# Performance work log

Hardware: AMD Instinct MI355X
Metric: run time of the kernel (lower is better)

## Reference

```python
import math
import jax, jax.numpy as jnp
import numpy as np

N_HEADS = 16


def setup_inputs() -> dict:
    key = jax.random.key(0)
    qkv = jax.random.normal(key, (4, 3072, 2048), dtype=jnp.float32)
    return {"qkv": qkv}


def reference(qkv) -> jnp.ndarray:
    bs, width, length = qkv.shape
    assert width % (3 * N_HEADS) == 0
    ch = width // (3 * N_HEADS)
    # [bs*H, 3*ch, T] -> q, k, v each [bs*H, ch, T]
    qkv_r = qkv.reshape(bs * N_HEADS, 3 * ch, length)
    q, k, v = qkv_r[:, :ch], qkv_r[:, ch:2 * ch], qkv_r[:, 2 * ch:]
    scale = 1.0 / math.sqrt(math.sqrt(ch))
    # scores: [bs*H, T, T]
    weight = jnp.einsum('bct,bcs->bts', q * scale, k * scale)
    weight = jax.nn.softmax(weight.astype(jnp.float32), axis=-1).astype(weight.dtype)
    a = jnp.einsum('bts,bcs->bct', weight, v)  # [bs*H, ch, T]
    return a.reshape(bs, N_HEADS * ch, length)
```

## Files before the change

kernel.cpp:

```cpp
#include <hip/hip_runtime.h>
#include <hip/hip_bf16.h>
#include <cstdint>
#include <cstddef>

typedef short bf16x8 __attribute__((ext_vector_type(8)));
typedef float f32x16 __attribute__((ext_vector_type(16)));
typedef unsigned int uint2v __attribute__((ext_vector_type(2)));

#define QSCALE 0.18033688011112043f

__device__ __forceinline__ short f2bf(float f) {
  union { __hip_bfloat16 b; short s; } u;
  u.b = __float2bfloat16(f);
  return u.s;
}

__device__ __forceinline__ float exp2v(float x) {
  float r;
  asm("v_exp_f32 %0, %1" : "=v"(r) : "v"(x));
  return r;
}

__device__ __forceinline__ unsigned int packbf2(float a, float b) {
  union { __hip_bfloat162 h; unsigned int w; } u;
  u.h = __float22bfloat162_rn(float2{a, b});
  return u.w;
}

__device__ __forceinline__ unsigned int fbits(float f) {
  union { float f; unsigned int u; } x; x.f = f; return x.u;
}
__device__ __forceinline__ float bfloat(unsigned int u) {
  union { unsigned int u; float f; } x; x.u = u; return x.f;
}

__device__ __forceinline__ float fmax_x32(float v) {
  const uint2v r = __builtin_amdgcn_permlane32_swap(fbits(v), fbits(v),
                                                    false, false);
  return fmaxf(bfloat(r[0]), bfloat(r[1]));
}
__device__ __forceinline__ float fadd_x32(float v) {
  const uint2v r = __builtin_amdgcn_permlane32_swap(fbits(v), fbits(v),
                                                    false, false);
  return bfloat(r[0]) + bfloat(r[1]);
}

__device__ __forceinline__ void gload16(const short* g, char* l) {
  __builtin_amdgcn_global_load_lds(
      (const __attribute__((address_space(1))) void*)g,
      (__attribute__((address_space(3))) void*)l, 16, 0, 0);
}

__global__ __launch_bounds__(256, 4) void qkv_prep_kernel(
    const float* __restrict__ qkv, short* __restrict__ Kt,
    short* __restrict__ Vb) {
  const int bh = blockIdx.x >> 5;
  const int s0 = (blockIdx.x & 31) << 6;
  const int tid = threadIdx.x;
  const int row = tid >> 2;
  const int part = tid & 3;
  __shared__ float lds[64 * 65];

  const size_t qb = (size_t)bh * (192 * 2048);

  {
    const float* src = qkv + qb + (size_t)(64 + row) * 2048 + s0 + part * 16;
#pragma unroll
    for (int k4 = 0; k4 < 4; ++k4) {
      float4 v = ((const float4*)src)[k4];
      float* p = &lds[row * 65 + part * 16 + k4 * 4];
      p[0] = v.x; p[1] = v.y; p[2] = v.z; p[3] = v.w;
    }
  }
  __syncthreads();
  {
    bf16x8 o0, o1;
#pragma unroll
    for (int k = 0; k < 8; ++k) o0[k] = f2bf(lds[(part * 16 + k) * 65 + row]);
#pragma unroll
    for (int k = 0; k < 8; ++k) o1[k] = f2bf(lds[(part * 16 + 8 + k) * 65 + row]);
    short* dst = Kt + ((size_t)bh * 2048 + s0 + row) * 64 + part * 16;
    *(bf16x8*)dst = o0;
    *(bf16x8*)(dst + 8) = o1;
  }
  {
    const float* src = qkv + qb + (size_t)(128 + row) * 2048 + s0 + part * 16;
    float a[16];
#pragma unroll
    for (int k4 = 0; k4 < 4; ++k4) {
      float4 v = ((const float4*)src)[k4];
      a[k4 * 4 + 0] = v.x; a[k4 * 4 + 1] = v.y;
      a[k4 * 4 + 2] = v.z; a[k4 * 4 + 3] = v.w;
    }
    bf16x8 o0, o1;
#pragma unroll
    for (int k = 0; k < 8; ++k) { o0[k] = f2bf(a[k]); o1[k] = f2bf(a[8 + k]); }
    short* dst = Vb + ((size_t)bh * 64 + row) * 2048 + s0 + part * 16;
    *(bf16x8*)dst = o0;
    *(bf16x8*)(dst + 8) = o1;
  }
}

__global__ __launch_bounds__(512, 4) void attn32_kernel(
    const float* __restrict__ qkv, const short* __restrict__ Kt,
    const short* __restrict__ Vb, float* __restrict__ out) {
  const int bid = blockIdx.x;
  const int vid = (bid & 7) * 64 + (bid >> 3);
  const int bh = vid >> 3;
  const int tblk = vid & 7;
  const int tid = threadIdx.x;
  const int wv = tid >> 6;
  const int lane = tid & 63;
  const int tl = lane & 31;
  const int hi = lane >> 5;
  const int t0w = tblk * 256 + wv * 32;

  __shared__ __align__(16) char smem[32768];

  const size_t qb = (size_t)bh * (192 * 2048);
  bf16x8 qf[4];
#pragma unroll
  for (int kc = 0; kc < 4; ++kc) {
#pragma unroll
    for (int j = 0; j < 8; ++j) {
      const int c = kc * 16 + hi * 8 + j;
      qf[kc][j] = f2bf(qkv[qb + (size_t)c * 2048 + t0w + tl] * QSCALE);
    }
  }

  f32x16 zv;
#pragma unroll
  for (int r = 0; r < 16; ++r) zv[r] = 0.f;

  f32x16 acc[2];
#pragma unroll
  for (int cb = 0; cb < 2; ++cb) acc[cb] = zv;

  float mrun = -1e30f;
  float lsum = 0.f;

  const int rsw = (tl & 7) * 16;
  int off[2][4];
#pragma unroll
  for (int x = 0; x < 2; ++x)
#pragma unroll
    for (int j = 0; j < 4; ++j)
      off[x][j] = (x * 32 + tl) * 128 + ((j * 32 + hi * 16) ^ rsw);

  const int srow = tid >> 3;
  const int sl = tid & 7;
  const short* kg = Kt + (size_t)bh * (2048 * 64) + (size_t)srow * 64 +
                    ((sl ^ (srow & 7)) * 8);
  const short* vg = Vb + ((size_t)bh * 64 + srow) * 2048 +
                    ((sl ^ (srow & 7)) * 8);
  const int ldb = wv * 1024;

  gload16(kg, smem + ldb);
  gload16(vg, smem + 8192 + ldb);

#pragma unroll 2
  for (int ch = 0; ch < 32; ++ch) {
    char* const Kls = smem + (ch & 1) * 16384;
    char* const Vls = Kls + 8192;

    __syncthreads();

    if (ch < 31) {
      char* const Knx = smem + ((ch + 1) & 1) * 16384;
      gload16(kg + (size_t)(ch + 1) * 4096, Knx + ldb);
      gload16(vg + (ch + 1) * 64, Knx + 8192 + ldb);
    }

    __builtin_amdgcn_s_setprio(1);
    f32x16 lg[2];
#pragma unroll
    for (int st = 0; st < 2; ++st) {
      bf16x8 ka = *(const bf16x8*)(Kls + off[st][0]);
      lg[st] = __builtin_amdgcn_mfma_f32_32x32x16_bf16(ka, qf[0], zv, 0, 0, 0);
#pragma unroll
      for (int kc = 1; kc < 4; ++kc) {
        ka = *(const bf16x8*)(Kls + off[st][kc]);
        lg[st] = __builtin_amdgcn_mfma_f32_32x32x16_bf16(ka, qf[kc], lg[st],
                                                         0, 0, 0);
      }
    }
    __builtin_amdgcn_s_setprio(0);

    float w[11];
#pragma unroll
    for (int i = 0; i < 5; ++i)
      w[i] = fmaxf(fmaxf(lg[0][3 * i], lg[0][3 * i + 1]), lg[0][3 * i + 2]);
    w[5] = fmaxf(fmaxf(lg[0][15], lg[1][0]), lg[1][1]);
#pragma unroll
    for (int i = 0; i < 4; ++i)
      w[6 + i] = fmaxf(fmaxf(lg[1][3 * i + 2], lg[1][3 * i + 3]),
                       lg[1][3 * i + 4]);
    w[10] = fmaxf(lg[1][14], lg[1][15]);
    const float x0 = fmaxf(fmaxf(w[0], w[1]), w[2]);
    const float x1 = fmaxf(fmaxf(w[3], w[4]), w[5]);
    const float x2 = fmaxf(fmaxf(w[6], w[7]), w[8]);
    const float x3 = fmaxf(w[9], w[10]);
    float cm = fmax_x32(fmaxf(fmaxf(x0, x1), fmaxf(x2, x3)));
    if (!__all(cm <= mrun + 8.0f)) {
      const float nm = fmaxf(mrun, cm);
      const float fac = exp2v(mrun - nm);
      mrun = nm;
      lsum *= fac;
#pragma unroll
      for (int cb = 0; cb < 2; ++cb)
#pragma unroll
        for (int r = 0; r < 16; ++r) acc[cb][r] *= fac;
    }

    float ps = 0.f;
#pragma unroll
    for (int st = 0; st < 2; ++st) {
#pragma unroll
      for (int r = 0; r < 16; ++r) lg[st][r] = exp2v(lg[st][r] - mrun);
#pragma unroll
      for (int r = 0; r < 8; ++r) ps += lg[st][2 * r] + lg[st][2 * r + 1];
    }
    lsum += ps;

    bf16x8 pa[4];
#pragma unroll
    for (int st = 0; st < 2; ++st) {
#pragma unroll
      for (int kl = 0; kl < 2; ++kl) {
        const unsigned int p0a = packbf2(lg[st][8 * kl + 0], lg[st][8 * kl + 1]);
        const unsigned int p0b = packbf2(lg[st][8 * kl + 2], lg[st][8 * kl + 3]);
        const unsigned int p1a = packbf2(lg[st][8 * kl + 4], lg[st][8 * kl + 5]);
        const unsigned int p1b = packbf2(lg[st][8 * kl + 6], lg[st][8 * kl + 7]);
        const unsigned int sa = hi ? p0a : p1a;
        const unsigned int sb = hi ? p0b : p1b;
        const unsigned int ra = __shfl_xor(sa, 32);
        const unsigned int rb = __shfl_xor(sb, 32);
        union { unsigned int w[4]; bf16x8 v; } u;
        u.w[0] = hi ? ra : p0a;
        u.w[1] = hi ? rb : p0b;
        u.w[2] = hi ? p1a : ra;
        u.w[3] = hi ? p1b : rb;
        pa[st * 2 + kl] = u.v;
      }
    }

    __builtin_amdgcn_s_setprio(1);
#pragma unroll
    for (int cb = 0; cb < 2; ++cb) {
#pragma unroll
      for (int ks = 0; ks < 4; ++ks) {
        const bf16x8 vb = *(const bf16x8*)(Vls + off[cb][ks]);
        acc[cb] = __builtin_amdgcn_mfma_f32_32x32x16_bf16(vb, pa[ks], acc[cb],
                                                          0, 0, 0);
      }
    }
    __builtin_amdgcn_s_setprio(0);
  }

  const float ls = fadd_x32(lsum);
  const float inv = 1.0f / ls;
#pragma unroll
  for (int cb = 0; cb < 2; ++cb) {
#pragma unroll
    for (int r = 0; r < 16; ++r) {
      const int c = cb * 32 + (r & 3) + 8 * (r >> 2) + 4 * hi;
      out[((size_t)bh * 64 + c) * 2048 + t0w + tl] = acc[cb][r] * inv;
    }
  }
}

extern "C" void kernel_launch(void* const* d_in, const int* in_sizes, int n_in,
                              void* d_out, int out_size, void* d_ws,
                              size_t ws_size, hipStream_t stream) {
  (void)in_sizes; (void)n_in; (void)out_size;
  const float* qkv = (const float*)d_in[0];
  float* out = (float*)d_out;
  const size_t kv_elems = (size_t)64 * 2048 * 64;
  if (ws_size < kv_elems * 2 * sizeof(short)) return;
  short* Kt = (short*)d_ws;
  short* Vb = Kt + kv_elems;
  hipLaunchKernelGGL(qkv_prep_kernel, dim3(2048), dim3(256), 0, stream,
                     qkv, Kt, Vb);
  hipLaunchKernelGGL(attn32_kernel, dim3(512), dim3(512), 0, stream,
                     qkv, Kt, Vb, out);
}
```

Measured before the change: 116.4 us.

## Split KV sequence across wave pairs and merge softmax partials in LDS

Each block now handles 128 queries instead of 256, with wave pairs splitting the KV chunks (even/odd) of the same query tile, and the grid doubles to 1024 blocks. Each iteration stages two K/V chunks into a 64KB double-buffered LDS, and at the end the odd wave writes its accumulator, running max and sum to LDS for the even wave to merge flash-style. This aims to raise parallelism and occupancy across CUs, at the cost of doubled K/V traffic per query, larger LDS use that may limit blocks per CU, and an extra merge step.

```diff
diff --git a/kernel.cpp b/kernel.cpp
--- a/kernel.cpp
+++ b/kernel.cpp
@@ -105,17 +105,19 @@
     const float* __restrict__ qkv, const short* __restrict__ Kt,
     const short* __restrict__ Vb, float* __restrict__ out) {
   const int bid = blockIdx.x;
-  const int vid = (bid & 7) * 64 + (bid >> 3);
-  const int bh = vid >> 3;
-  const int tblk = vid & 7;
+  const int vid = (bid & 7) * 128 + (bid >> 3);
+  const int bh = vid >> 4;
+  const int tblk = vid & 15;
   const int tid = threadIdx.x;
   const int wv = tid >> 6;
+  const int tt = wv >> 1;
+  const int par = wv & 1;
   const int lane = tid & 63;
   const int tl = lane & 31;
   const int hi = lane >> 5;
-  const int t0w = tblk * 256 + wv * 32;
-
-  __shared__ __align__(16) char smem[32768];
+  const int t0w = tblk * 128 + tt * 32;
+
+  __shared__ __align__(16) char smem[65536];
 
   const size_t qb = (size_t)bh * (192 * 2048);
   bf16x8 qf[4];
@@ -155,21 +157,28 @@
                     ((sl ^ (srow & 7)) * 8);
   const int ldb = wv * 1024;
 
-  gload16(kg, smem + ldb);
-  gload16(vg, smem + 8192 + ldb);
-
-#pragma unroll 2
-  for (int ch = 0; ch < 32; ++ch) {
-    char* const Kls = smem + (ch & 1) * 16384;
-    char* const Vls = Kls + 8192;
+  gload16(kg, smem + 0 * 8192 + ldb);
+  gload16(kg + 4096, smem + 1 * 8192 + ldb);
+  gload16(vg, smem + 2 * 8192 + ldb);
+  gload16(vg + 64, smem + 3 * 8192 + ldb);
+
+  for (int p = 0; p < 16; ++p) {
+    char* const set = smem + (p & 1) * 32768;
 
     __syncthreads();
 
-    if (ch < 31) {
-      char* const Knx = smem + ((ch + 1) & 1) * 16384;
-      gload16(kg + (size_t)(ch + 1) * 4096, Knx + ldb);
-      gload16(vg + (ch + 1) * 64, Knx + 8192 + ldb);
-    }
+    if (p < 15) {
+      char* const ns = smem + ((p + 1) & 1) * 32768;
+      const size_t k0 = (size_t)(2 * p + 2) * 4096;
+      const int v0 = (2 * p + 2) * 64;
+      gload16(kg + k0, ns + 0 * 8192 + ldb);
+      gload16(kg + k0 + 4096, ns + 1 * 8192 + ldb);
+      gload16(vg + v0, ns + 2 * 8192 + ldb);
+      gload16(vg + v0 + 64, ns + 3 * 8192 + ldb);
+    }
+
+    char* const Kls = set + par * 8192;
+    char* const Vls = set + 16384 + par * 8192;
 
     __builtin_amdgcn_s_setprio(1);
     f32x16 lg[2];
@@ -257,14 +266,39 @@
     __builtin_amdgcn_s_setprio(0);
   }
 
-  const float ls = fadd_x32(lsum);
-  const float inv = 1.0f / ls;
-#pragma unroll
-  for (int cb = 0; cb < 2; ++cb) {
-#pragma unroll
-    for (int r = 0; r < 16; ++r) {
-      const int c = cb * 32 + (r & 3) + 8 * (r >> 2) + 4 * hi;
-      out[((size_t)bh * 64 + c) * 2048 + t0w + tl] = acc[cb][r] * inv;
+  __syncthreads();
+  float* const accb = (float*)smem;
+  float* const mlb = (float*)(smem + 32768);
+  if (par == 1) {
+    float* ap = accb + (tt * 64 + lane) * 32;
+    union { f32x16 v; float4 q[4]; } u;
+#pragma unroll
+    for (int cb = 0; cb < 2; ++cb) {
+      u.v = acc[cb];
+#pragma unroll
+      for (int i = 0; i < 4; ++i) ((float4*)ap)[cb * 4 + i] = u.q[i];
+    }
+    mlb[(tt * 64 + lane) * 2 + 0] = mrun;
+    mlb[(tt * 64 + lane) * 2 + 1] = lsum;
+  }
+  __syncthreads();
+  if (par == 0) {
+    const float m1 = mlb[(tt * 64 + lane) * 2 + 0];
+    const float l1 = mlb[(tt * 64 + lane) * 2 + 1];
+    const float m = fmaxf(mrun, m1);
+    const float f0 = exp2v(mrun - m);
+    const float f1 = exp2v(m1 - m);
+    const float ls = fadd_x32(lsum * f0 + l1 * f1);
+    const float inv = 1.0f / ls;
+    const float* ap = accb + (tt * 64 + lane) * 32;
+#pragma unroll
+    for (int cb = 0; cb < 2; ++cb) {
+#pragma unroll
+      for (int r = 0; r < 16; ++r) {
+        const int c = cb * 32 + (r & 3) + 8 * (r >> 2) + 4 * hi;
+        const float o = (acc[cb][r] * f0 + ap[cb * 16 + r] * f1) * inv;
+        out[((size_t)bh * 64 + c) * 2048 + t0w + tl] = o;
+      }
     }
   }
 }
@@ -281,6 +315,6 @@
   short* Vb = Kt + kv_elems;
   hipLaunchKernelGGL(qkv_prep_kernel, dim3(2048), dim3(256), 0, stream,
                      qkv, Kt, Vb);
-  hipLaunchKernelGGL(attn32_kernel, dim3(512), dim3(512), 0, stream,
+  hipLaunchKernelGGL(attn32_kernel, dim3(1024), dim3(512), 0, stream,
                      qkv, Kt, Vb, out);
 }
```

Result: slower. 122.5 us (+5.3%).
